# Performance work log

Measured on AMD Instinct MI355X. Metric: run time of the kernel, lower is better.

The kernel has to match this reference:

```python
import jax, jax.numpy as jnp
import numpy as np

B, N, E, D, OUT, L = 4, 10000, 160000, 128, 64, 4
NEG = 0.01  # LeakyReLU slope

def lrelu(x):
    return jnp.where(x > 0, x, NEG * x)

def setup_inputs() -> dict:
    key = jax.random.key(0)
    ks = jax.random.split(key, 20)
    s = 0.05
    inp = {
        "x": jax.random.normal(ks[0], (B, N * 3), dtype=jnp.float32),
        "edge_index": jax.random.randint(ks[1], (2, E), 0, N, dtype=jnp.int32),
        # f0: Linear(3, D)
        "w0": jax.random.normal(ks[2], (3, D), dtype=jnp.float32) * s,
        "b0": jax.random.normal(ks[3], (D,), dtype=jnp.float32) * s,
        # per-layer params stacked on leading L axis
        "ew1": jax.random.normal(ks[4], (L, 2 * D + 1, D), dtype=jnp.float32) * s,
        "eb1": jax.random.normal(ks[5], (L, D), dtype=jnp.float32) * s,
        "ew2": jax.random.normal(ks[6], (L, D, D), dtype=jnp.float32) * s,
        "eb2": jax.random.normal(ks[7], (L, D), dtype=jnp.float32) * s,
        "cw": jax.random.normal(ks[8], (L, D, 1), dtype=jnp.float32) * s,
        "cb": jax.random.normal(ks[9], (L, 1), dtype=jnp.float32) * s,
        "nw1": jax.random.normal(ks[10], (L, 2 * D, D), dtype=jnp.float32) * s,
        "nb1": jax.random.normal(ks[11], (L, D), dtype=jnp.float32) * s,
        "nw2": jax.random.normal(ks[12], (L, D, D), dtype=jnp.float32) * s,
        "nb2": jax.random.normal(ks[13], (L, D), dtype=jnp.float32) * s,
        # project: Linear(D, OUT)
        "wp": jax.random.normal(ks[14], (D, OUT), dtype=jnp.float32) * s,
        "bp": jax.random.normal(ks[15], (OUT,), dtype=jnp.float32) * s,
    }
    return inp

def reference(x, edge_index, w0, b0, ew1, eb1, ew2, eb2, cw, cb, nw1, nb1, nw2, nb2, wp, bp):
    b = x.shape[0]
    n = x.shape[1] // 3
    pos = x.reshape(b, n, 3)            # coordinates [B,N,3]
    h = lrelu(pos @ w0 + b0)            # node features [B,N,D]
    row, col = edge_index[0], edge_index[1]
    # per-node in-edge counts (same for all layers/batches); scatter_mean -> 0 for empty nodes
    cnt = jnp.zeros((n,), x.dtype).at[col].add(1.0)
    denom = jnp.maximum(cnt, 1.0)[None, :, None]
    for i in range(L):
        rel = pos[:, row] - pos[:, col]                          # [B,E,3]
        dist_sq = jnp.sum(rel * rel, axis=-1, keepdims=True)     # [B,E,1]
        edge_in = jnp.concatenate([h[:, row], h[:, col], dist_sq], axis=-1)  # [B,E,2D+1]
        msg = lrelu(lrelu(edge_in @ ew1[i] + eb1[i]) @ ew2[i] + eb2[i])       # [B,E,D]
        aggr = jnp.zeros((b, n, msg.shape[-1]), msg.dtype).at[:, col].add(msg) / denom  # scatter_mean
        coord_update = jnp.tanh(aggr @ cw[i] + cb[i])            # [B,N,1]
        pos = pos + coord_update * 0.1
        node_in = jnp.concatenate([h, aggr], axis=-1)            # [B,N,2D]
        h = h + lrelu(lrelu(node_in @ nw1[i] + nb1[i]) @ nw2[i] + nb2[i])
    return lrelu(h.mean(axis=1) @ wp + bp)                       # [B,OUT]
```

## Files before the change

kernel.cpp:

```cpp
#include <hip/hip_runtime.h>
#include <hip/hip_bf16.h>
#include <math.h>

#define BB   4
#define NN   10000
#define NP   10112
#define EE   160000
#define DD   128
#define OUTD 64
#define LL   4
#define NEGS 0.01f
#define MSTR 136
#define RSF  34

typedef __attribute__((ext_vector_type(8))) short   short8;
typedef __attribute__((ext_vector_type(4))) float   floatx4;
typedef __attribute__((ext_vector_type(4))) uint    uintx4;

__device__ __forceinline__ float lrelu(float x) { return fmaxf(x, NEGS * x); }
__device__ __forceinline__ ushort f2bf(float x) {
    uint u = __builtin_bit_cast(uint, x);
    return (ushort)((u + 0x7FFFu + ((u >> 16) & 1u)) >> 16);
}
__device__ __forceinline__ float bf2f(ushort u) {
    uint v = ((uint)u) << 16;
    return __builtin_bit_cast(float, v);
}
__device__ __forceinline__ float bcf(uint u) { return __builtin_bit_cast(float, u); }

__global__ void k_cvtw_all(const float* __restrict__ ew1, const float* __restrict__ ew2,
                           const float* __restrict__ nw1, const float* __restrict__ nw2,
                           ushort* __restrict__ wtopf, ushort* __restrict__ wmidf,
                           ushort* __restrict__ ew2f, ushort* __restrict__ nw1f,
                           ushort* __restrict__ nw2f) {
    int tid = blockIdx.x * 256 + threadIdx.x;
    const float* src; ushort* dst; int pitch, nks, loc;
    if (tid < 8192)       { src = ew1;                     dst = wtopf; pitch = 257; nks = 4; loc = tid; }
    else if (tid < 16384) { src = ew1 + (size_t)128 * DD;  dst = wmidf; pitch = 257; nks = 4; loc = tid - 8192; }
    else if (tid < 24576) { src = ew2;                     dst = ew2f;  pitch = 128; nks = 4; loc = tid - 16384; }
    else if (tid < 40960) { src = nw1;                     dst = nw1f;  pitch = 256; nks = 8; loc = tid - 24576; }
    else                  { src = nw2;                     dst = nw2f;  pitch = 128; nks = 4; loc = tid - 40960; }
    int lane = loc & 63;
    int nt   = (loc >> 6) & 7;
    int ks   = (loc >> 9) % nks;
    int l    = loc / (nks * 512);
    int quad = lane >> 4, l16 = lane & 15;
    int n = nt * 16 + l16;
    const float* s = src + (size_t)l * pitch * DD;
    ushort* d = dst + (size_t)loc * 8;
    #pragma unroll
    for (int j = 0; j < 8; ++j)
        d[j] = f2bf(s[(size_t)(ks * 32 + quad * 8 + j) * DD + n]);
}

__global__ void k_h0(const float* __restrict__ x, const float* __restrict__ w0,
                     const float* __restrict__ b0, ushort* __restrict__ hb) {
    int idx = blockIdx.x * 256 + threadIdx.x;
    if (idx >= BB * NP * DD) return;
    int d  = idx & (DD - 1);
    int bn = idx >> 7;
    int n  = bn % NP, b = bn / NP;
    float v = 0.0f;
    if (n < NN) {
        const float* p = x + ((size_t)b * NN + n) * 3;
        v = lrelu(b0[d] + p[0] * w0[d] + p[1] * w0[DD + d] + p[2] * w0[2 * DD + d]);
    }
    hb[idx] = f2bf(v);
}

__global__ void k_count(const int* __restrict__ col, float* __restrict__ cnt,
                        int* __restrict__ ecnt) {
    int e = blockIdx.x * blockDim.x + threadIdx.x;
    if (e < EE) {
        int c = col[e];
        atomicAdd(&cnt[c], 1.0f);
        atomicAdd(&ecnt[c], 1);
    }
}

__global__ __launch_bounds__(256) void k_scan(const int* __restrict__ ecnt,
                                              int* __restrict__ cursor) {
    __shared__ int s_sum[256];
    int t = threadIdx.x;
    int base = t * 40;
    int s = 0;
    for (int i = 0; i < 40; ++i) {
        int n = base + i;
        if (n < NN) s += ecnt[n];
    }
    s_sum[t] = s;
    __syncthreads();
    if (t == 0) {
        int a = 0;
        for (int i = 0; i < 256; ++i) { int v = s_sum[i]; s_sum[i] = a; a += v; }
    }
    __syncthreads();
    int a = s_sum[t];
    for (int i = 0; i < 40; ++i) {
        int n = base + i;
        if (n < NN) { cursor[n] = a; a += ecnt[n]; }
    }
}

__global__ void k_place(const int* __restrict__ row, const int* __restrict__ col,
                        int* __restrict__ cursor,
                        int* __restrict__ rowS, int* __restrict__ colS) {
    int e = blockIdx.x * blockDim.x + threadIdx.x;
    if (e >= EE) return;
    int c = col[e];
    int p = atomicAdd(&cursor[c], 1);
    rowS[p] = row[e];
    colS[p] = c;
}

__global__ __launch_bounds__(256) void k_pq(
    const ushort* __restrict__ hb, const ushort* __restrict__ wtf,
    const ushort* __restrict__ wmf, const float* __restrict__ b1,
    ushort* __restrict__ P, ushort* __restrict__ Q)
{
    __shared__ __align__(16) ushort s_out[64 * MSTR];
    const int g = blockIdx.x;
    const int b = (g >> 1) & 3;
    const int n0 = ((g >> 3) * 2 + (g & 1)) * 64;
    const int t = threadIdx.x;
    const int w = t >> 6, lane = t & 63, quad = lane >> 4, l16 = lane & 15;
    const int rw = w * 16;
    const int nw = n0 + rw;

    const ushort* hptr = hb + ((size_t)b * NP + nw + l16) * DD;
    float b1r[8];
    #pragma unroll
    for (int nt = 0; nt < 8; ++nt) b1r[nt] = b1[nt * 16 + l16];

    const short8* wt = (const short8*)wtf;
    const short8* wm = (const short8*)wmf;

    #pragma unroll
    for (int pass = 0; pass < 2; ++pass) {
        floatx4 ap[8];
        #pragma unroll
        for (int nt = 0; nt < 8; ++nt)
            #pragma unroll
            for (int r = 0; r < 4; ++r) ap[nt][r] = pass ? b1r[nt] : 0.0f;
        const short8* wv = pass ? wm : wt;
        #pragma unroll
        for (int ks = 0; ks < 4; ++ks) {
            short8 bf[8];
            #pragma unroll
            for (int nt = 0; nt < 8; ++nt) bf[nt] = wv[(ks * 8 + nt) * 64 + lane];
            short8 af = *(const short8*)(hptr + ks * 32 + quad * 8);
            #pragma unroll
            for (int nt = 0; nt < 8; ++nt)
                ap[nt] = __builtin_amdgcn_mfma_f32_16x16x32_bf16(af, bf[nt], ap[nt], 0, 0, 0);
        }
        #pragma unroll
        for (int nt = 0; nt < 8; ++nt)
            #pragma unroll
            for (int r = 0; r < 4; ++r)
                s_out[(rw + quad * 4 + r) * MSTR + nt * 16 + l16] = f2bf(ap[nt][r]);
        ushort* dst = pass ? Q : P;
        #pragma unroll
        for (int i = 0; i < 4; ++i) {
            int row = rw + i * 4 + quad;
            short8 v = *(const short8*)&s_out[row * MSTR + l16 * 8];
            *(short8*)(dst + ((size_t)b * NP + n0 + row) * DD + l16 * 8) = v;
        }
    }
}

__global__ __launch_bounds__(256, 4) void k_edge(
    const float* __restrict__ pos,
    const ushort* __restrict__ P, const ushort* __restrict__ Q,
    const int* __restrict__ rowS, const int* __restrict__ colS,
    const float* __restrict__ w1last,
    const ushort* __restrict__ w2f, const float* __restrict__ b2,
    float* __restrict__ aggr)
{
    __shared__ __align__(16) int    s_col[128];
    __shared__ __align__(16) float  s_ds[128];
    __shared__ __align__(16) float  s_red[128 * RSF];

    const int g    = blockIdx.x;
    const int b    = (g >> 1) & 3;
    const int tile = (g >> 3) * 2 + (g & 1);
    const int e0   = tile * 128;
    const int t    = threadIdx.x;
    const int w    = t >> 6, lane = t & 63;
    const int quad = lane >> 4, l16 = lane & 15;
    const int ew   = w * 32;

    const ushort* pp[2];
    const ushort* qp[2];
    #pragma unroll
    for (int mt = 0; mt < 2; ++mt) {
        int el = e0 + ew + mt * 16 + l16;
        pp[mt] = P + ((size_t)b * NP + rowS[el]) * DD;
        qp[mt] = Q + ((size_t)b * NP + colS[el]) * DD;
    }

    uintx4 pf[2][4], qf[2][4];
    #pragma unroll
    for (int ks = 0; ks < 4; ++ks) {
        const int koff = ks * 32 + quad * 8;
        #pragma unroll
        for (int mt = 0; mt < 2; ++mt) {
            pf[mt][ks] = *(const uintx4*)(pp[mt] + koff);
            qf[mt][ks] = *(const uintx4*)(qp[mt] + koff);
        }
    }

    if (t < 128) {
        int e = e0 + t;
        int r = rowS[e], c = colS[e];
        s_col[t] = c;
        const float* pr = pos + ((size_t)b * NN + r) * 3;
        const float* pc = pos + ((size_t)b * NN + c) * 3;
        float dx = pr[0] - pc[0], dy = pr[1] - pc[1], dz = pr[2] - pc[2];
        s_ds[t] = dx * dx + dy * dy + dz * dz;
    }
    __syncthreads();

    const int rh    = lane >> 5;
    const int colL  = lane & 31;
    const int rbase = ew + rh * 16;
    int bmask = 0, cid0;
    {
        int prev = s_col[rbase];
        cid0 = prev;
        #pragma unroll
        for (int r2 = 1; r2 < 16; ++r2) {
            int c = s_col[rbase + r2];
            if (c != prev) bmask |= (1 << r2);
            prev = c;
        }
    }

    float dsv[2];
    #pragma unroll
    for (int mt = 0; mt < 2; ++mt) dsv[mt] = s_ds[ew + mt * 16 + l16];

    uintx4 mid[2][4];
    #pragma unroll
    for (int ks = 0; ks < 4; ++ks) {
        const int koff = ks * 32 + quad * 8;
        floatx4 wl0 = *(const floatx4*)(w1last + koff);
        floatx4 wl1 = *(const floatx4*)(w1last + koff + 4);
        float wl[8] = {wl0[0], wl0[1], wl0[2], wl0[3], wl1[0], wl1[1], wl1[2], wl1[3]};
        #pragma unroll
        for (int mt = 0; mt < 2; ++mt) {
            #pragma unroll
            for (int i = 0; i < 4; ++i) {
                uint pv = pf[mt][ks][i], qv = qf[mt][ks][i];
                float vlo = lrelu(bcf(pv << 16) + bcf(qv << 16) + dsv[mt] * wl[2 * i]);
                float vhi = lrelu(bcf(pv & 0xFFFF0000u) + bcf(qv & 0xFFFF0000u) + dsv[mt] * wl[2 * i + 1]);
                mid[mt][ks][i] = __builtin_amdgcn_perm(
                    __builtin_bit_cast(uint, vhi), __builtin_bit_cast(uint, vlo), 0x07060302u);
            }
        }
    }

    float* aggr_bd = aggr + (size_t)b * NP * DD;

    const short8* w2v = (const short8*)w2f;
    #pragma unroll
    for (int ph = 0; ph < 2; ++ph) {
        float b2r4[4];
        #pragma unroll
        for (int ntl = 0; ntl < 4; ++ntl) b2r4[ntl] = b2[(ph * 4 + ntl) * 16 + l16];

        floatx4 acc[2][4];
        #pragma unroll
        for (int mt = 0; mt < 2; ++mt)
            #pragma unroll
            for (int ntl = 0; ntl < 4; ++ntl)
                #pragma unroll
                for (int r = 0; r < 4; ++r) acc[mt][ntl][r] = b2r4[ntl];

        #pragma unroll
        for (int ks = 0; ks < 4; ++ks) {
            short8 bf[4];
            #pragma unroll
            for (int ntl = 0; ntl < 4; ++ntl)
                bf[ntl] = w2v[(ks * 8 + ph * 4 + ntl) * 64 + lane];
            #pragma unroll
            for (int mt = 0; mt < 2; ++mt) {
                short8 af = __builtin_bit_cast(short8, mid[mt][ks]);
                #pragma unroll
                for (int ntl = 0; ntl < 4; ++ntl)
                    acc[mt][ntl] = __builtin_amdgcn_mfma_f32_16x16x32_bf16(af, bf[ntl], acc[mt][ntl], 0, 0, 0);
            }
        }

        #pragma unroll
        for (int sp = 0; sp < 2; ++sp) {
            #pragma unroll
            for (int mt = 0; mt < 2; ++mt)
                #pragma unroll
                for (int j = 0; j < 2; ++j) {
                    const int ntl = sp * 2 + j;
                    #pragma unroll
                    for (int r = 0; r < 4; ++r)
                        s_red[(ew + mt * 16 + quad * 4 + r) * RSF + j * 16 + l16] =
                            lrelu(acc[mt][ntl][r]);
                }

            const int d = ph * 64 + sp * 32 + colL;
            float* ab = aggr_bd + d;
            float run = 0.0f;
            int cid = cid0;
            #pragma unroll
            for (int r = 0; r < 16; ++r) {
                float v = s_red[(rbase + r) * RSF + colL];
                if (bmask & (1 << r)) {
                    atomicAdd(ab + (size_t)cid * DD, run);
                    run = 0.0f;
                    cid = s_col[rbase + r];
                }
                run += v;
            }
            atomicAdd(ab + (size_t)cid * DD, run);
        }
    }
}

__global__ __launch_bounds__(256) void k_node(
    ushort* hb, float* aggr, const float* __restrict__ cnt,
    const float* __restrict__ cw, const float* __restrict__ cb,
    const ushort* __restrict__ w1f, const float* __restrict__ b1,
    const ushort* __restrict__ w2f, const float* __restrict__ b2,
    float* __restrict__ pos,
    int do_pq,
    const ushort* __restrict__ wtn, const ushort* __restrict__ wmn,
    const float* __restrict__ b1n,
    ushort* __restrict__ P, ushort* __restrict__ Q)
{
    __shared__ __align__(16) ushort s_mid[64 * MSTR];
    __shared__ __align__(16) ushort s_ho[64 * MSTR];

    const int g    = blockIdx.x;
    const int b    = (g >> 1) & 3;
    const int n0   = ((g >> 3) * 2 + (g & 1)) * 64;
    const int t    = threadIdx.x;
    const int w    = t >> 6, lane = t & 63;
    const int quad = lane >> 4, l16 = lane & 15;
    const int rw   = w * 16;
    const int nw   = n0 + rw;

    #pragma unroll
    for (int i = 0; i < 4; ++i) {
        int row = rw + i * 4 + quad;
        short8 v = *(const short8*)(hb + ((size_t)b * NP + n0 + row) * DD + l16 * 8);
        *(short8*)&s_ho[row * MSTR + l16 * 8] = v;
    }

    float* aptr = aggr + ((size_t)b * NP + nw + l16) * DD;
    float inv = 0.0f;
    {
        int node = nw + l16;
        if (node < NN) { float dn = cnt[node]; inv = 1.0f / fmaxf(dn, 1.0f); }
    }
    float b1r[8], b2r[8];
    #pragma unroll
    for (int nt = 0; nt < 8; ++nt) {
        int d = nt * 16 + l16;
        b1r[nt] = b1[d]; b2r[nt] = b2[d];
    }

    floatx4 acc[8];
    #pragma unroll
    for (int nt = 0; nt < 8; ++nt)
        #pragma unroll
        for (int r = 0; r < 4; ++r) acc[nt][r] = b1r[nt];

    float cwacc = 0.0f;
    const floatx4 zero4 = {0.0f, 0.0f, 0.0f, 0.0f};
    const short8* w1v = (const short8*)w1f;
    #pragma unroll
    for (int ks = 0; ks < 8; ++ks) {
        short8 bf[8];
        #pragma unroll
        for (int nt = 0; nt < 8; ++nt) bf[nt] = w1v[(ks * 8 + nt) * 64 + lane];
        const int koff = (ks & 3) * 32 + quad * 8;
        if (ks < 4) {
            short8 af = *(const short8*)(&s_ho[(rw + l16) * MSTR + koff]);
            #pragma unroll
            for (int nt = 0; nt < 8; ++nt)
                acc[nt] = __builtin_amdgcn_mfma_f32_16x16x32_bf16(af, bf[nt], acc[nt], 0, 0, 0);
        } else {
            floatx4 cw0 = *(const floatx4*)(cw + koff);
            floatx4 cw1 = *(const floatx4*)(cw + koff + 4);
            floatx4 a0 = *(const floatx4*)(aptr + koff);
            floatx4 a1 = *(const floatx4*)(aptr + koff + 4);
            *(floatx4*)(aptr + koff)     = zero4;
            *(floatx4*)(aptr + koff + 4) = zero4;
            short8 af;
            #pragma unroll
            for (int j = 0; j < 4; ++j) {
                float v = a0[j] * inv;
                af[j] = (short)f2bf(v);
                cwacc += v * cw0[j];
            }
            #pragma unroll
            for (int j = 0; j < 4; ++j) {
                float v = a1[j] * inv;
                af[4 + j] = (short)f2bf(v);
                cwacc += v * cw1[j];
            }
            #pragma unroll
            for (int nt = 0; nt < 8; ++nt)
                acc[nt] = __builtin_amdgcn_mfma_f32_16x16x32_bf16(af, bf[nt], acc[nt], 0, 0, 0);
        }
    }

    {
        float full = cwacc;
        full += __shfl_xor(full, 16);
        full += __shfl_xor(full, 32);
        int node = nw + l16;
        if (quad == 0 && node < NN) {
            float cu = 0.1f * tanhf(full + cb[0]);
            float* pp = pos + ((size_t)b * NN + node) * 3;
            pp[0] += cu; pp[1] += cu; pp[2] += cu;
        }
    }

    #pragma unroll
    for (int nt = 0; nt < 8; ++nt)
        #pragma unroll
        for (int r = 0; r < 4; ++r)
            s_mid[(rw + quad * 4 + r) * MSTR + nt * 16 + l16] = f2bf(lrelu(acc[nt][r]));

    floatx4 acc2[8];
    #pragma unroll
    for (int nt = 0; nt < 8; ++nt)
        #pragma unroll
        for (int r = 0; r < 4; ++r) acc2[nt][r] = b2r[nt];

    const short8* w2v = (const short8*)w2f;
    #pragma unroll
    for (int ks = 0; ks < 4; ++ks) {
        short8 bf[8];
        #pragma unroll
        for (int nt = 0; nt < 8; ++nt) bf[nt] = w2v[(ks * 8 + nt) * 64 + lane];
        short8 af = *(const short8*)(&s_mid[(rw + l16) * MSTR + ks * 32 + quad * 8]);
        #pragma unroll
        for (int nt = 0; nt < 8; ++nt)
            acc2[nt] = __builtin_amdgcn_mfma_f32_16x16x32_bf16(af, bf[nt], acc2[nt], 0, 0, 0);
    }

    #pragma unroll
    for (int nt = 0; nt < 8; ++nt)
        #pragma unroll
        for (int r = 0; r < 4; ++r) {
            int row = rw + quad * 4 + r;
            float hold = bf2f(s_ho[row * MSTR + nt * 16 + l16]);
            float hv = hold + lrelu(acc2[nt][r]);
            s_mid[row * MSTR + nt * 16 + l16] = f2bf(hv);
        }

    #pragma unroll
    for (int i = 0; i < 4; ++i) {
        int row = rw + i * 4 + quad;
        int n = n0 + row;
        short8 v = *(const short8*)&s_mid[row * MSTR + l16 * 8];
        if (n < NN)
            *(short8*)(hb + ((size_t)b * NP + n) * DD + l16 * 8) = v;
    }

    if (do_pq) {
        const short8* wt = (const short8*)wtn;
        const short8* wm = (const short8*)wmn;
        float b1nr[8];
        #pragma unroll
        for (int nt = 0; nt < 8; ++nt) b1nr[nt] = b1n[nt * 16 + l16];

        #pragma unroll
        for (int pass = 0; pass < 2; ++pass) {
            floatx4 ap[8];
            #pragma unroll
            for (int nt = 0; nt < 8; ++nt)
                #pragma unroll
                for (int r = 0; r < 4; ++r) ap[nt][r] = pass ? b1nr[nt] : 0.0f;
            const short8* wv = pass ? wm : wt;
            #pragma unroll
            for (int ks = 0; ks < 4; ++ks) {
                short8 bf[8];
                #pragma unroll
                for (int nt = 0; nt < 8; ++nt) bf[nt] = wv[(ks * 8 + nt) * 64 + lane];
                short8 af = *(const short8*)(&s_mid[(rw + l16) * MSTR + ks * 32 + quad * 8]);
                #pragma unroll
                for (int nt = 0; nt < 8; ++nt)
                    ap[nt] = __builtin_amdgcn_mfma_f32_16x16x32_bf16(af, bf[nt], ap[nt], 0, 0, 0);
            }
            #pragma unroll
            for (int nt = 0; nt < 8; ++nt)
                #pragma unroll
                for (int r = 0; r < 4; ++r)
                    s_ho[(rw + quad * 4 + r) * MSTR + nt * 16 + l16] = f2bf(ap[nt][r]);
            ushort* dst = pass ? Q : P;
            #pragma unroll
            for (int i = 0; i < 4; ++i) {
                int row = rw + i * 4 + quad;
                short8 v = *(const short8*)&s_ho[row * MSTR + l16 * 8];
                *(short8*)(dst + ((size_t)b * NP + n0 + row) * DD + l16 * 8) = v;
            }
        }
    }
}

#define NPC 50
__global__ void k_mean(const ushort* __restrict__ hb, float* __restrict__ hm) {
    int b  = blockIdx.y;
    int n0 = blockIdx.x * NPC;
    int d  = threadIdx.x;
    float s = 0.0f;
    for (int n = n0; n < n0 + NPC; ++n) s += bf2f(hb[((size_t)b * NP + n) * DD + d]);
    atomicAdd(&hm[b * DD + d], s);
}

__global__ void k_proj(const float* __restrict__ hm, const float* __restrict__ wp,
                       const float* __restrict__ bp, float* __restrict__ out) {
    int t = threadIdx.x;
    int b = t >> 6, o = t & (OUTD - 1);
    float s = 0.0f;
    for (int d2 = 0; d2 < DD; ++d2) s += hm[b * DD + d2] * wp[d2 * OUTD + o];
    s = s * (1.0f / NN) + bp[o];
    out[b * OUTD + o] = lrelu(s);
}

extern "C" void kernel_launch(void* const* d_in, const int* in_sizes, int n_in,
                              void* d_out, int out_size, void* d_ws, size_t ws_size,
                              hipStream_t stream) {
    (void)in_sizes; (void)n_in; (void)out_size; (void)ws_size;
    const float* x   = (const float*)d_in[0];
    const int*   ei  = (const int*)d_in[1];
    const float* w0  = (const float*)d_in[2];
    const float* b0  = (const float*)d_in[3];
    const float* ew1 = (const float*)d_in[4];
    const float* eb1 = (const float*)d_in[5];
    const float* ew2 = (const float*)d_in[6];
    const float* eb2 = (const float*)d_in[7];
    const float* cw  = (const float*)d_in[8];
    const float* cb  = (const float*)d_in[9];
    const float* nw1 = (const float*)d_in[10];
    const float* nb1 = (const float*)d_in[11];
    const float* nw2 = (const float*)d_in[12];
    const float* nb2 = (const float*)d_in[13];
    const float* wp  = (const float*)d_in[14];
    const float* bp  = (const float*)d_in[15];
    const int* row = ei;
    const int* col = ei + EE;

    const size_t HSZ = (size_t)BB * NP * DD;
    float* ws   = (float*)d_ws;
    float* aggr = ws;
    float* pos  = aggr + HSZ;
    float* cnt  = pos + (size_t)BB * NN * 3;
    float* hm   = cnt + NN;
    ushort* hb    = (ushort*)(hm + 512);
    ushort* Pb    = hb + HSZ;
    ushort* Qb    = Pb + HSZ;
    ushort* wtopf = Qb + HSZ;
    ushort* wmidf = wtopf + (size_t)LL * 16384;
    ushort* ew2f  = wmidf + (size_t)LL * 16384;
    ushort* nw1f  = ew2f + (size_t)LL * 16384;
    ushort* nw2f  = nw1f + (size_t)LL * 32768;
    int* ecnt   = (int*)(nw2f + (size_t)LL * 16384);
    int* cursor = ecnt + NN;
    int* rowS   = cursor + NN;
    int* colS   = rowS + EE;

    hipMemcpyAsync(pos, x, sizeof(float) * (size_t)BB * NN * 3,
                   hipMemcpyDeviceToDevice, stream);
    hipMemsetAsync(cnt, 0, sizeof(float) * NN, stream);
    hipMemsetAsync(ecnt, 0, sizeof(int) * NN, stream);
    hipMemsetAsync(hm, 0, sizeof(float) * BB * DD, stream);
    hipMemsetAsync(aggr, 0, sizeof(float) * HSZ, stream);

    k_cvtw_all<<<192, 256, 0, stream>>>(ew1, ew2, nw1, nw2,
                                        wtopf, wmidf, ew2f, nw1f, nw2f);

    k_h0<<<((int)HSZ + 255) / 256, 256, 0, stream>>>(x, w0, b0, hb);
    k_count<<<(EE + 255) / 256, 256, 0, stream>>>(col, cnt, ecnt);
    k_scan<<<1, 256, 0, stream>>>(ecnt, cursor);
    k_place<<<(EE + 255) / 256, 256, 0, stream>>>(row, col, cursor, rowS, colS);

    k_pq<<<(NP / 64) * BB, 256, 0, stream>>>(hb, wtopf, wmidf, eb1, Pb, Qb);

    for (int i = 0; i < LL; ++i) {
        k_edge<<<(EE / 128) * BB, 256, 0, stream>>>(
            pos, Pb, Qb, rowS, colS,
            ew1 + (size_t)i * 257 * DD + (size_t)256 * DD,
            ew2f + (size_t)i * 16384,
            eb2 + (size_t)i * DD,
            aggr);
        int nx = (i < LL - 1) ? (i + 1) : i;
        k_node<<<(NP / 64) * BB, 256, 0, stream>>>(
            hb, aggr, cnt,
            cw + (size_t)i * DD, cb + i,
            nw1f + (size_t)i * 32768, nb1 + (size_t)i * DD,
            nw2f + (size_t)i * 16384, nb2 + (size_t)i * DD,
            pos,
            (i < LL - 1) ? 1 : 0,
            wtopf + (size_t)nx * 16384, wmidf + (size_t)nx * 16384,
            eb1 + (size_t)nx * DD,
            Pb, Qb);
    }

    k_mean<<<dim3(NN / NPC, BB), DD, 0, stream>>>(hb, hm);
    k_proj<<<1, 256, 0, stream>>>(hm, wp, bp, (float*)d_out);
}
```

Before: 579.0 us.

## Make edge kernel loop over multiple tiles with prefetched next-tile gathers

Each edge-kernel block now processes TPB consecutive 128-edge tiles instead of one. It double-buffers the column indices and squared distances in shared memory and issues the next tile's P/Q row gathers and position loads while the current tile's MLP and atomic scatter run. This is meant to hide gather latency and amortize per-block setup such as the bias loads. In exchange the grid shrinks tenfold, the launch-bounds occupancy hint drops from 4 to 2, and register pressure rises, so fewer waves are left to hide latency and load balance at the tail gets worse.

```diff
diff --git a/kernel.cpp b/kernel.cpp
--- a/kernel.cpp
+++ b/kernel.cpp
@@ -12,6 +12,7 @@
 #define NEGS 0.01f
 #define MSTR 136
 #define RSF  34
+#define TPB  10
 
 typedef __attribute__((ext_vector_type(8))) short   short8;
 typedef __attribute__((ext_vector_type(4))) float   floatx4;
@@ -168,7 +169,7 @@
     }
 }
 
-__global__ __launch_bounds__(256, 4) void k_edge(
+__global__ __launch_bounds__(256, 2) void k_edge(
     const float* __restrict__ pos,
     const ushort* __restrict__ P, const ushort* __restrict__ Q,
     const int* __restrict__ rowS, const int* __restrict__ colS,
@@ -176,150 +177,190 @@
     const ushort* __restrict__ w2f, const float* __restrict__ b2,
     float* __restrict__ aggr)
 {
-    __shared__ __align__(16) int    s_col[128];
-    __shared__ __align__(16) float  s_ds[128];
+    __shared__ __align__(16) int    s_col[2][128];
+    __shared__ __align__(16) float  s_ds[2][128];
     __shared__ __align__(16) float  s_red[128 * RSF];
 
     const int g    = blockIdx.x;
-    const int b    = (g >> 1) & 3;
-    const int tile = (g >> 3) * 2 + (g & 1);
-    const int e0   = tile * 128;
+    const int b    = g & 3;
+    const int t0   = (g >> 2) * TPB;
     const int t    = threadIdx.x;
     const int w    = t >> 6, lane = t & 63;
     const int quad = lane >> 4, l16 = lane & 15;
     const int ew   = w * 32;
-
-    const ushort* pp[2];
-    const ushort* qp[2];
-    #pragma unroll
-    for (int mt = 0; mt < 2; ++mt) {
-        int el = e0 + ew + mt * 16 + l16;
-        pp[mt] = P + ((size_t)b * NP + rowS[el]) * DD;
-        qp[mt] = Q + ((size_t)b * NP + colS[el]) * DD;
-    }
+    const int rh     = lane >> 5;
+    const int colL   = lane & 31;
+    const int rbaseL = ew + rh * 16;
+
+    const ushort* Pb_ = P + (size_t)b * NP * DD;
+    const ushort* Qb_ = Q + (size_t)b * NP * DD;
+    const float*  posb = pos + (size_t)b * NN * 3;
+    float* aggr_bd = aggr + (size_t)b * NP * DD;
+
+    float b2r[8];
+    #pragma unroll
+    for (int nt = 0; nt < 8; ++nt) b2r[nt] = b2[nt * 16 + l16];
 
     uintx4 pf[2][4], qf[2][4];
-    #pragma unroll
-    for (int ks = 0; ks < 4; ++ks) {
-        const int koff = ks * 32 + quad * 8;
+    {
+        const ushort* pp[2];
+        const ushort* qp[2];
         #pragma unroll
         for (int mt = 0; mt < 2; ++mt) {
-            pf[mt][ks] = *(const uintx4*)(pp[mt] + koff);
-            qf[mt][ks] = *(const uintx4*)(qp[mt] + koff);
-        }
-    }
-
+            int el = t0 * 128 + ew + mt * 16 + l16;
+            pp[mt] = Pb_ + (size_t)rowS[el] * DD;
+            qp[mt] = Qb_ + (size_t)colS[el] * DD;
+        }
+        #pragma unroll
+        for (int ks = 0; ks < 4; ++ks) {
+            const int koff = ks * 32 + quad * 8;
+            #pragma unroll
+            for (int mt = 0; mt < 2; ++mt) {
+                pf[mt][ks] = *(const uintx4*)(pp[mt] + koff);
+                qf[mt][ks] = *(const uintx4*)(qp[mt] + koff);
+            }
+        }
+    }
     if (t < 128) {
-        int e = e0 + t;
+        int e = t0 * 128 + t;
         int r = rowS[e], c = colS[e];
-        s_col[t] = c;
-        const float* pr = pos + ((size_t)b * NN + r) * 3;
-        const float* pc = pos + ((size_t)b * NN + c) * 3;
+        s_col[0][t] = c;
+        const float* pr = posb + (size_t)r * 3;
+        const float* pc = posb + (size_t)c * 3;
         float dx = pr[0] - pc[0], dy = pr[1] - pc[1], dz = pr[2] - pc[2];
-        s_ds[t] = dx * dx + dy * dy + dz * dz;
+        s_ds[0][t] = dx * dx + dy * dy + dz * dz;
     }
     __syncthreads();
 
-    const int rh    = lane >> 5;
-    const int colL  = lane & 31;
-    const int rbase = ew + rh * 16;
-    int bmask = 0, cid0;
-    {
-        int prev = s_col[rbase];
-        cid0 = prev;
-        #pragma unroll
-        for (int r2 = 1; r2 < 16; ++r2) {
-            int c = s_col[rbase + r2];
-            if (c != prev) bmask |= (1 << r2);
-            prev = c;
-        }
-    }
-
-    float dsv[2];
-    #pragma unroll
-    for (int mt = 0; mt < 2; ++mt) dsv[mt] = s_ds[ew + mt * 16 + l16];
-
-    uintx4 mid[2][4];
-    #pragma unroll
-    for (int ks = 0; ks < 4; ++ks) {
-        const int koff = ks * 32 + quad * 8;
-        floatx4 wl0 = *(const floatx4*)(w1last + koff);
-        floatx4 wl1 = *(const floatx4*)(w1last + koff + 4);
-        float wl[8] = {wl0[0], wl0[1], wl0[2], wl0[3], wl1[0], wl1[1], wl1[2], wl1[3]};
-        #pragma unroll
-        for (int mt = 0; mt < 2; ++mt) {
-            #pragma unroll
-            for (int i = 0; i < 4; ++i) {
-                uint pv = pf[mt][ks][i], qv = qf[mt][ks][i];
-                float vlo = lrelu(bcf(pv << 16) + bcf(qv << 16) + dsv[mt] * wl[2 * i]);
-                float vhi = lrelu(bcf(pv & 0xFFFF0000u) + bcf(qv & 0xFFFF0000u) + dsv[mt] * wl[2 * i + 1]);
-                mid[mt][ks][i] = __builtin_amdgcn_perm(
-                    __builtin_bit_cast(uint, vhi), __builtin_bit_cast(uint, vlo), 0x07060302u);
-            }
-        }
-    }
-
-    float* aggr_bd = aggr + (size_t)b * NP * DD;
-
-    const short8* w2v = (const short8*)w2f;
-    #pragma unroll
-    for (int ph = 0; ph < 2; ++ph) {
-        float b2r4[4];
-        #pragma unroll
-        for (int ntl = 0; ntl < 4; ++ntl) b2r4[ntl] = b2[(ph * 4 + ntl) * 16 + l16];
-
-        floatx4 acc[2][4];
-        #pragma unroll
-        for (int mt = 0; mt < 2; ++mt)
-            #pragma unroll
-            for (int ntl = 0; ntl < 4; ++ntl)
-                #pragma unroll
-                for (int r = 0; r < 4; ++r) acc[mt][ntl][r] = b2r4[ntl];
-
+    #pragma unroll 1
+    for (int it = 0; it < TPB; ++it) {
+        const int  cur  = it & 1;
+        const bool more = (it + 1 < TPB);
+
+        int bmask = 0, cid0;
+        {
+            int prev = s_col[cur][rbaseL];
+            cid0 = prev;
+            #pragma unroll
+            for (int r2 = 1; r2 < 16; ++r2) {
+                int c = s_col[cur][rbaseL + r2];
+                if (c != prev) bmask |= (1 << r2);
+                prev = c;
+            }
+        }
+        float dsv[2];
+        #pragma unroll
+        for (int mt = 0; mt < 2; ++mt) dsv[mt] = s_ds[cur][ew + mt * 16 + l16];
+
+        const ushort* np[2];
+        const ushort* nq[2];
+        if (more) {
+            #pragma unroll
+            for (int mt = 0; mt < 2; ++mt) {
+                int el = (t0 + it + 1) * 128 + ew + mt * 16 + l16;
+                np[mt] = Pb_ + (size_t)rowS[el] * DD;
+                nq[mt] = Qb_ + (size_t)colS[el] * DD;
+            }
+        }
+
+        uintx4 mid[2][4];
         #pragma unroll
         for (int ks = 0; ks < 4; ++ks) {
-            short8 bf[4];
-            #pragma unroll
-            for (int ntl = 0; ntl < 4; ++ntl)
-                bf[ntl] = w2v[(ks * 8 + ph * 4 + ntl) * 64 + lane];
+            const int koff = ks * 32 + quad * 8;
+            floatx4 wl0 = *(const floatx4*)(w1last + koff);
+            floatx4 wl1 = *(const floatx4*)(w1last + koff + 4);
+            float wl[8] = {wl0[0], wl0[1], wl0[2], wl0[3], wl1[0], wl1[1], wl1[2], wl1[3]};
             #pragma unroll
             for (int mt = 0; mt < 2; ++mt) {
-                short8 af = __builtin_bit_cast(short8, mid[mt][ks]);
+                #pragma unroll
+                for (int i = 0; i < 4; ++i) {
+                    uint pv = pf[mt][ks][i], qv = qf[mt][ks][i];
+                    float vlo = lrelu(bcf(pv << 16) + bcf(qv << 16) + dsv[mt] * wl[2 * i]);
+                    float vhi = lrelu(bcf(pv & 0xFFFF0000u) + bcf(qv & 0xFFFF0000u) + dsv[mt] * wl[2 * i + 1]);
+                    mid[mt][ks][i] = __builtin_amdgcn_perm(
+                        __builtin_bit_cast(uint, vhi), __builtin_bit_cast(uint, vlo), 0x07060302u);
+                }
+            }
+        }
+
+        if (more) {
+            #pragma unroll
+            for (int ks = 0; ks < 4; ++ks) {
+                const int koff = ks * 32 + quad * 8;
+                #pragma unroll
+                for (int mt = 0; mt < 2; ++mt) {
+                    pf[mt][ks] = *(const uintx4*)(np[mt] + koff);
+                    qf[mt][ks] = *(const uintx4*)(nq[mt] + koff);
+                }
+            }
+            if (t < 128) {
+                int e = (t0 + it + 1) * 128 + t;
+                int r = rowS[e], c = colS[e];
+                s_col[cur ^ 1][t] = c;
+                const float* pr = posb + (size_t)r * 3;
+                const float* pc = posb + (size_t)c * 3;
+                float dx = pr[0] - pc[0], dy = pr[1] - pc[1], dz = pr[2] - pc[2];
+                s_ds[cur ^ 1][t] = dx * dx + dy * dy + dz * dz;
+            }
+        }
+
+        const short8* w2v = (const short8*)w2f;
+        #pragma unroll
+        for (int ph = 0; ph < 2; ++ph) {
+            floatx4 acc[2][4];
+            #pragma unroll
+            for (int mt = 0; mt < 2; ++mt)
                 #pragma unroll
                 for (int ntl = 0; ntl < 4; ++ntl)
-                    acc[mt][ntl] = __builtin_amdgcn_mfma_f32_16x16x32_bf16(af, bf[ntl], acc[mt][ntl], 0, 0, 0);
-            }
-        }
-
-        #pragma unroll
-        for (int sp = 0; sp < 2; ++sp) {
-            #pragma unroll
-            for (int mt = 0; mt < 2; ++mt)
-                #pragma unroll
-                for (int j = 0; j < 2; ++j) {
-                    const int ntl = sp * 2 + j;
                     #pragma unroll
-                    for (int r = 0; r < 4; ++r)
-                        s_red[(ew + mt * 16 + quad * 4 + r) * RSF + j * 16 + l16] =
-                            lrelu(acc[mt][ntl][r]);
+                    for (int r = 0; r < 4; ++r) acc[mt][ntl][r] = b2r[ph * 4 + ntl];
+
+            #pragma unroll
+            for (int ks = 0; ks < 4; ++ks) {
+                short8 bf[4];
+                #pragma unroll
+                for (int ntl = 0; ntl < 4; ++ntl)
+                    bf[ntl] = w2v[(ks * 8 + ph * 4 + ntl) * 64 + lane];
+                #pragma unroll
+                for (int mt = 0; mt < 2; ++mt) {
+                    short8 af = __builtin_bit_cast(short8, mid[mt][ks]);
+                    #pragma unroll
+                    for (int ntl = 0; ntl < 4; ++ntl)
+                        acc[mt][ntl] = __builtin_amdgcn_mfma_f32_16x16x32_bf16(af, bf[ntl], acc[mt][ntl], 0, 0, 0);
                 }
-
-            const int d = ph * 64 + sp * 32 + colL;
-            float* ab = aggr_bd + d;
-            float run = 0.0f;
-            int cid = cid0;
-            #pragma unroll
-            for (int r = 0; r < 16; ++r) {
-                float v = s_red[(rbase + r) * RSF + colL];
-                if (bmask & (1 << r)) {
-                    atomicAdd(ab + (size_t)cid * DD, run);
-                    run = 0.0f;
-                    cid = s_col[rbase + r];
+            }
+
+            #pragma unroll
+            for (int sp = 0; sp < 2; ++sp) {
+                #pragma unroll
+                for (int mt = 0; mt < 2; ++mt)
+                    #pragma unroll
+                    for (int j = 0; j < 2; ++j) {
+                        const int ntl = sp * 2 + j;
+                        #pragma unroll
+                        for (int r = 0; r < 4; ++r)
+                            s_red[(ew + mt * 16 + quad * 4 + r) * RSF + j * 16 + l16] =
+                                lrelu(acc[mt][ntl][r]);
+                    }
+
+                const int d = ph * 64 + sp * 32 + colL;
+                float* ab = aggr_bd + d;
+                float run = 0.0f;
+                int cid = cid0;
+                #pragma unroll
+                for (int r = 0; r < 16; ++r) {
+                    float v = s_red[(rbaseL + r) * RSF + colL];
+                    if (bmask & (1 << r)) {
+                        atomicAdd(ab + (size_t)cid * DD, run);
+                        run = 0.0f;
+                        cid = s_col[cur][rbaseL + r];
+                    }
+                    run += v;
                 }
-                run += v;
-            }
-            atomicAdd(ab + (size_t)cid * DD, run);
-        }
+                atomicAdd(ab + (size_t)cid * DD, run);
+            }
+        }
+        __syncthreads();
     }
 }
 
@@ -588,7 +629,7 @@
     k_pq<<<(NP / 64) * BB, 256, 0, stream>>>(hb, wtopf, wmidf, eb1, Pb, Qb);
 
     for (int i = 0; i < LL; ++i) {
-        k_edge<<<(EE / 128) * BB, 256, 0, stream>>>(
+        k_edge<<<(EE / 128 / TPB) * BB, 256, 0, stream>>>(
             pos, Pb, Qb, rowS, colS,
             ew1 + (size_t)i * 257 * DD + (size_t)256 * DD,
             ew2f + (size_t)i * 16384,
```

New measurement: 928.6 us. 1.6x slower.

## Accumulate edge messages per destination node in LDS before writing to global

Applied to the files above, without the earlier changes.

The edge kernel used to stage activated messages in a shared scratch buffer, then run a 16-row segmented scan that issued global float atomics. It now reduces runs of equal destination node directly in MFMA accumulator registers. Those partial sums are atomically added into a small per-tile LDS accumulator covering up to 24 consecutive destination nodes. After a barrier, the tile writes its interior nodes to global memory with plain stores, and uses atomics only for the boundary nodes it shares with neighbouring tiles. The aim is to cut global atomic traffic and the shared scratch round trip, at the cost of extra LDS zeroing, LDS atomics and a fallback global-atomic path when the column span exceeds 24 nodes.

```diff
diff --git a/kernel.cpp b/kernel.cpp
--- a/kernel.cpp
+++ b/kernel.cpp
@@ -11,7 +11,7 @@
 #define LL   4
 #define NEGS 0.01f
 #define MSTR 136
-#define RSF  34
+#define NACC 24
 
 typedef __attribute__((ext_vector_type(8))) short   short8;
 typedef __attribute__((ext_vector_type(4))) float   floatx4;
@@ -178,7 +178,7 @@
 {
     __shared__ __align__(16) int    s_col[128];
     __shared__ __align__(16) float  s_ds[128];
-    __shared__ __align__(16) float  s_red[128 * RSF];
+    __shared__ __align__(16) float  s_nacc[NACC][DD];
 
     const int g    = blockIdx.x;
     const int b    = (g >> 1) & 3;
@@ -197,7 +197,6 @@
         pp[mt] = P + ((size_t)b * NP + rowS[el]) * DD;
         qp[mt] = Q + ((size_t)b * NP + colS[el]) * DD;
     }
-
     uintx4 pf[2][4], qf[2][4];
     #pragma unroll
     for (int ks = 0; ks < 4; ++ks) {
@@ -218,22 +217,25 @@
         float dx = pr[0] - pc[0], dy = pr[1] - pc[1], dz = pr[2] - pc[2];
         s_ds[t] = dx * dx + dy * dy + dz * dz;
     }
+    {
+        const floatx4 z4 = {0.0f, 0.0f, 0.0f, 0.0f};
+        floatx4* z = (floatx4*)&s_nacc[0][0];
+        #pragma unroll
+        for (int i = 0; i < 3; ++i) z[t + i * 256] = z4;
+    }
     __syncthreads();
 
-    const int rh    = lane >> 5;
-    const int colL  = lane & 31;
-    const int rbase = ew + rh * 16;
-    int bmask = 0, cid0;
-    {
-        int prev = s_col[rbase];
-        cid0 = prev;
-        #pragma unroll
-        for (int r2 = 1; r2 < 16; ++r2) {
-            int c = s_col[rbase + r2];
-            if (c != prev) bmask |= (1 << r2);
-            prev = c;
-        }
-    }
+    const int  c_first = s_col[0];
+    const int  c_last  = s_col[127];
+    const int  span    = c_last - c_first + 1;
+    const bool lds_ok  = (span <= NACC);
+
+    int colreg[2][4];
+    #pragma unroll
+    for (int mt = 0; mt < 2; ++mt)
+        #pragma unroll
+        for (int r = 0; r < 4; ++r)
+            colreg[mt][r] = s_col[ew + mt * 16 + quad * 4 + r];
 
     float dsv[2];
     #pragma unroll
@@ -292,33 +294,43 @@
         }
 
         #pragma unroll
-        for (int sp = 0; sp < 2; ++sp) {
-            #pragma unroll
-            for (int mt = 0; mt < 2; ++mt)
+        for (int mt = 0; mt < 2; ++mt) {
+            #pragma unroll
+            for (int ntl = 0; ntl < 4; ++ntl) {
+                const int d = (ph * 4 + ntl) * 16 + l16;
+                float run = lrelu(acc[mt][ntl][0]);
+                int   cid = colreg[mt][0];
                 #pragma unroll
-                for (int j = 0; j < 2; ++j) {
-                    const int ntl = sp * 2 + j;
-                    #pragma unroll
-                    for (int r = 0; r < 4; ++r)
-                        s_red[(ew + mt * 16 + quad * 4 + r) * RSF + j * 16 + l16] =
-                            lrelu(acc[mt][ntl][r]);
+                for (int r = 1; r < 4; ++r) {
+                    float v = lrelu(acc[mt][ntl][r]);
+                    int   c = colreg[mt][r];
+                    if (c != cid) {
+                        if (lds_ok) atomicAdd(&s_nacc[cid - c_first][d], run);
+                        else        atomicAdd(aggr_bd + (size_t)cid * DD + d, run);
+                        cid = c; run = v;
+                    } else {
+                        run += v;
+                    }
                 }
-
-            const int d = ph * 64 + sp * 32 + colL;
-            float* ab = aggr_bd + d;
-            float run = 0.0f;
-            int cid = cid0;
-            #pragma unroll
-            for (int r = 0; r < 16; ++r) {
-                float v = s_red[(rbase + r) * RSF + colL];
-                if (bmask & (1 << r)) {
-                    atomicAdd(ab + (size_t)cid * DD, run);
-                    run = 0.0f;
-                    cid = s_col[rbase + r];
-                }
-                run += v;
+                if (lds_ok) atomicAdd(&s_nacc[cid - c_first][d], run);
+                else        atomicAdd(aggr_bd + (size_t)cid * DD + d, run);
             }
-            atomicAdd(ab + (size_t)cid * DD, run);
+        }
+    }
+
+    __syncthreads();
+    if (lds_ok) {
+        const bool shf = (e0 > 0)        && (colS[e0 - 1]   == c_first);
+        const bool shl = (e0 + 128 < EE) && (colS[e0 + 128] == c_last);
+        const int total = span * DD;
+        for (int idx = t; idx < total; idx += 256) {
+            int nl = idx >> 7, d = idx & 127;
+            float v = s_nacc[nl][d];
+            int node = c_first + nl;
+            bool sh = (nl == 0 && shf) || (nl == span - 1 && shl);
+            float* p = aggr_bd + (size_t)node * DD + d;
+            if (sh) atomicAdd(p, v);
+            else    *p = v;
         }
     }
 }
```

New measurement: 876.1 us. +51.3%, slower.
